# Optimization experiments

Hardware: AMD Instinct MI355X
Metric: run time of the kernel (lower is better)

## Reference

```python
import jax, jax.numpy as jnp
import numpy as np

NUM_HEADS = 16

def _rms_norm(x):
    # F.rms_norm over last dim, eps = dtype machine epsilon (torch default eps=None)
    eps = jnp.finfo(jnp.float32).eps
    ms = jnp.mean(jnp.square(x.astype(jnp.float32)), axis=-1, keepdims=True)
    return (x.astype(jnp.float32) * jax.lax.rsqrt(ms + eps)).astype(x.dtype)

def _rotary_tables(T, head_dim):
    # inv_freq = (1/1024)**linspace(0,1,head_dim//4), padded with zeros to head_dim//2
    quarter = head_dim // 4
    inv_freq = (1.0 / 1024.0) ** jnp.linspace(0.0, 1.0, quarter, dtype=jnp.float32)
    inv_freq = jnp.concatenate([inv_freq, jnp.zeros(quarter, dtype=jnp.float32)])
    t = jnp.arange(T, dtype=jnp.float32)
    theta = t[:, None] * inv_freq[None, :]          # [T, head_dim//2]
    return jnp.cos(theta), jnp.sin(theta)

def _rotary(x, cos, sin):
    # x: [B, T, H, hd]; rotate in fp32, cast back
    xf = x.astype(jnp.float32)
    x1, x2 = jnp.split(xf, 2, axis=-1)
    c = cos[None, :, None, :]
    s = sin[None, :, None, :]
    y1 = x1 * c + x2 * s
    y2 = -x1 * s + x2 * c
    return jnp.concatenate([y1, y2], axis=-1).astype(x.dtype)

def setup_inputs() -> dict:
    key = jax.random.key(0)
    ks = jax.random.split(key, 7)
    B, T, D = 1, 2048, 1024
    sc = 1.0 / np.sqrt(D)
    return {
        "x": jax.random.normal(ks[0], (B, T, D), jnp.float32),
        "vi": jax.random.normal(ks[1], (B, T, D), jnp.float32),
        "Wq": jax.random.normal(ks[2], (D, D), jnp.float32) * sc,
        "Wk": jax.random.normal(ks[3], (D, D), jnp.float32) * sc,
        "Wv": jax.random.normal(ks[4], (D, D), jnp.float32) * sc,
        "Wproj": jax.random.normal(ks[5], (D, D), jnp.float32) * sc,
        "lambdas": jnp.array([0.5, 0.5], jnp.float32),
    }

def reference(x, vi, Wq, Wk, Wv, Wproj, lambdas):
    B, T, D = x.shape
    H = NUM_HEADS
    hd = D // H
    q = (x @ Wq.T).reshape(B, T, H, hd)
    k = (x @ Wk.T).reshape(B, T, H, hd)
    v = (x @ Wv.T).reshape(B, T, H, hd)
    # value residual: lambda-mixed v
    v = lambdas[0] * v + lambdas[1] * vi.reshape(B, T, H, hd)
    q, k = _rms_norm(q), _rms_norm(k)
    cos, sin = _rotary_tables(T, hd)
    q, k = _rotary(q, cos, sin), _rotary(k, cos, sin)
    # causal attention, default flex_attention scale = 1/sqrt(head_dim)
    scores = jnp.einsum('bthd,bshd->bhts', q, k) / jnp.sqrt(jnp.float32(hd))
    causal = jnp.tril(jnp.ones((T, T), dtype=bool))
    scores = jnp.where(causal[None, None], scores, jnp.float32(-1e30))
    attn = jax.nn.softmax(scores, axis=-1)
    y = jnp.einsum('bhts,bshd->bthd', attn, v).reshape(B, T, D)
    return y @ Wproj.T
```

## Files before the change

kernel.cpp:

```cpp
#include <hip/hip_runtime.h>
#include <math.h>

#define T_SEQ 2048
#define D_MODEL 1024
#define NH 16
#define HD 64

typedef unsigned short ushort_t;
typedef unsigned int uint_t;
typedef short short8 __attribute__((ext_vector_type(8)));
typedef float floatx4 __attribute__((ext_vector_type(4)));

__device__ __forceinline__ ushort_t f2bf(float f) {
    uint_t u = __float_as_uint(f);
    u += 0x7FFFu + ((u >> 16) & 1u);
    return (ushort_t)(u >> 16);
}
__device__ __forceinline__ uint_t pack2(float a, float b) {
    return (uint_t)f2bf(a) | ((uint_t)f2bf(b) << 16);
}
__device__ __forceinline__ void gload16(const ushort_t* g, ushort_t* l) {
    __builtin_amdgcn_global_load_lds(
        (const __attribute__((address_space(1))) void*)g,
        (__attribute__((address_space(3))) void*)l, 16, 0, 0);
}

__global__ __launch_bounds__(256) void to_bf16(
        const float* __restrict__ x,  const float* __restrict__ wq,
        const float* __restrict__ wk, const float* __restrict__ wv,
        const float* __restrict__ wp,
        ushort_t* __restrict__ xb,  ushort_t* __restrict__ wqb,
        ushort_t* __restrict__ wkb, ushort_t* __restrict__ wvb,
        ushort_t* __restrict__ wpb)
{
    size_t i = (size_t)blockIdx.x * 256 + threadIdx.x;
    const float* src; ushort_t* dst; size_t off;
    if (i < 262144)      { src = x;  dst = xb;  off = i; }
    else if (i < 393216) { src = wq; dst = wqb; off = i - 262144; }
    else if (i < 524288) { src = wk; dst = wkb; off = i - 393216; }
    else if (i < 655360) { src = wv; dst = wvb; off = i - 524288; }
    else                 { src = wp; dst = wpb; off = i - 655360; }
    float4 f0 = ((const float4*)src)[off * 2];
    float4 f1 = ((const float4*)src)[off * 2 + 1];
    uint4 u;
    u.x = pack2(f0.x, f0.y); u.y = pack2(f0.z, f0.w);
    u.z = pack2(f1.x, f1.y); u.w = pack2(f1.z, f1.w);
    ((uint4*)dst)[off] = u;
}

__global__ __launch_bounds__(256) void gemm_qkv(
        const ushort_t* __restrict__ xb,
        const ushort_t* __restrict__ Wqb, const ushort_t* __restrict__ Wkb,
        const ushort_t* __restrict__ Wvb,
        const float* __restrict__ vi, const float* __restrict__ lam,
        ushort_t* __restrict__ qb, ushort_t* __restrict__ kb,
        ushort_t* __restrict__ vbt)
{
    const int z = blockIdx.z;
    const ushort_t* __restrict__ W = (z == 0) ? Wqb : (z == 1) ? Wkb : Wvb;
    const int d  = blockIdx.y * 8 + blockIdx.x;
    const int ly = (d & 7) * 4 + (d >> 6);
    const int lx = (d >> 3) & 7;
    const int row0 = ly * 64;
    const int col0 = lx * 128;

    __shared__ ushort_t As[2 * 64 * 64];
    __shared__ ushort_t Bs[2 * 128 * 64];

    const int tid = threadIdx.x;
    const int wave = tid >> 6, lane = tid & 63;
    const int wm = wave >> 1, wn = wave & 1;
    const int l15 = lane & 15, quad = lane >> 4;
    const int srow  = tid >> 3;
    const int sslot = (tid & 7) ^ (srow & 7);

    floatx4 acc[2][4];
    #pragma unroll
    for (int i = 0; i < 2; ++i)
        #pragma unroll
        for (int j = 0; j < 4; ++j)
            acc[i][j] = (floatx4){0.f, 0.f, 0.f, 0.f};

    auto stageAB = [&](int k0, int p) {
        ushort_t* Ap = As + p * 4096;
        ushort_t* Bp = Bs + p * 8192;
        #pragma unroll
        for (int c = 0; c < 2; ++c)
            gload16(xb + (size_t)(row0 + c * 32 + srow) * D_MODEL + k0 + sslot * 8,
                    Ap + c * 2048 + tid * 8);
        #pragma unroll
        for (int c = 0; c < 4; ++c)
            gload16(W + (size_t)(col0 + c * 32 + srow) * D_MODEL + k0 + sslot * 8,
                    Bp + c * 2048 + tid * 8);
    };

    stageAB(0, 0);
    int cur = 0;
    for (int k0 = 0; k0 < D_MODEL; k0 += 64) {
        asm volatile("s_waitcnt vmcnt(0)" ::: "memory");
        __builtin_amdgcn_s_barrier();
        const ushort_t* Ac = As + cur * 4096;
        const ushort_t* Bc = Bs + cur * 8192;
        short8 a[2][2], b[2][4];
        #pragma unroll
        for (int kh = 0; kh < 2; ++kh) {
            const int slot = ((kh * 4 + quad) ^ (l15 & 7)) << 3;
            #pragma unroll
            for (int i = 0; i < 2; ++i)
                a[kh][i] = *(const short8*)(Ac + (32 * wm + i * 16 + l15) * 64 + slot);
            #pragma unroll
            for (int j = 0; j < 4; ++j)
                b[kh][j] = *(const short8*)(Bc + (64 * wn + j * 16 + l15) * 64 + slot);
        }
        __builtin_amdgcn_sched_barrier(0);
        if (k0 + 64 < D_MODEL) stageAB(k0 + 64, cur ^ 1);
        __builtin_amdgcn_sched_barrier(0);
        #pragma unroll
        for (int kh = 0; kh < 2; ++kh)
            #pragma unroll
            for (int i = 0; i < 2; ++i)
                #pragma unroll
                for (int j = 0; j < 4; ++j)
                    acc[i][j] = __builtin_amdgcn_mfma_f32_16x16x32_bf16(a[kh][i], b[kh][j], acc[i][j], 0, 0, 0);
        cur ^= 1;
    }

    if (z < 2) {
        ushort_t* __restrict__ o = (z == 0) ? qb : kb;
        const float oscale = (z == 0) ? 0.125f : 1.0f;
        const int hbase = col0 + 64 * wn;
        const float eps = 1.1920929e-7f;
        const float fr = exp2f(-10.0f * (float)l15 / 15.0f);
        #pragma unroll
        for (int i = 0; i < 2; ++i)
            #pragma unroll
            for (int r = 0; r < 4; ++r) {
                const int t = row0 + 32 * wm + i * 16 + quad * 4 + r;
                float v0 = acc[i][0][r], v1 = acc[i][1][r];
                float v2 = acc[i][2][r], v3 = acc[i][3][r];
                float ss = v0 * v0 + v1 * v1 + v2 * v2 + v3 * v3;
                ss += __shfl_xor(ss, 1);
                ss += __shfl_xor(ss, 2);
                ss += __shfl_xor(ss, 4);
                ss += __shfl_xor(ss, 8);
                const float sc = rsqrtf(ss * (1.0f / 64.0f) + eps);
                v0 *= sc; v1 *= sc; v2 *= sc; v3 *= sc;
                const float th = (float)t * fr;
                const float cs = cosf(th), sn = sinf(th);
                const float y0 = v0 * cs + v2 * sn;
                const float y2 = v2 * cs - v0 * sn;
                const size_t rb = (size_t)t * D_MODEL + hbase;
                o[rb +  0 + l15] = f2bf(y0 * oscale);
                o[rb + 16 + l15] = f2bf(v1 * oscale);
                o[rb + 32 + l15] = f2bf(y2 * oscale);
                o[rb + 48 + l15] = f2bf(v3 * oscale);
            }
    } else {
        const float l0 = lam[0], l1 = lam[1];
        #pragma unroll
        for (int i = 0; i < 2; ++i)
            #pragma unroll
            for (int j = 0; j < 4; ++j) {
                const int tb = row0 + 32 * wm + i * 16 + quad * 4;
                const int jj = col0 + 64 * wn + j * 16 + l15;
                float b0 = l0 * acc[i][j][0] + l1 * vi[(size_t)(tb + 0) * D_MODEL + jj];
                float b1 = l0 * acc[i][j][1] + l1 * vi[(size_t)(tb + 1) * D_MODEL + jj];
                float b2 = l0 * acc[i][j][2] + l1 * vi[(size_t)(tb + 2) * D_MODEL + jj];
                float b3 = l0 * acc[i][j][3] + l1 * vi[(size_t)(tb + 3) * D_MODEL + jj];
                uint2 u;
                u.x = pack2(b0, b1);
                u.y = pack2(b2, b3);
                *(uint2*)(vbt + (size_t)jj * T_SEQ + tb) = u;
            }
    }
}

__global__ __launch_bounds__(256) void attn(
        const ushort_t* __restrict__ qb, const ushort_t* __restrict__ kb,
        const ushort_t* __restrict__ vbt, ushort_t* __restrict__ yb,
        float* __restrict__ Opart, float* __restrict__ Lpart)
{
    const int h = blockIdx.x;
    const int x = blockIdx.y;
    int qt, ct_begin, ct_end, pidx;
    if (x < 28) {
        qt = 27 - (x >> 1);
        const int w = qt + 1;
        const int c0 = (w + 1) >> 1;
        if ((x & 1) == 0) { ct_begin = 0;  ct_end = c0; }
        else              { ct_begin = c0; ct_end = w;  }
        pidx = h * 40 + 12 + (qt - 14) * 2 + (x & 1);
    } else if (x < 40) {
        const int xx = x - 28;
        qt = 28 + xx / 3;
        const int c = xx % 3;
        const int w = qt + 1;
        const int b0 = (w + 2) / 3;
        const int b1 = (2 * w + 2) / 3;
        ct_begin = (c == 0) ? 0  : (c == 1) ? b0 : b1;
        ct_end   = (c == 0) ? b0 : (c == 1) ? b1 : w;
        pidx = h * 40 + (qt - 28) * 3 + c;
    } else {
        qt = 53 - x;
        ct_begin = 0; ct_end = qt + 1;
        pidx = -1;
    }
    const int t0 = qt * 64;

    __shared__ ushort_t Ks[2 * 64 * 64];
    __shared__ ushort_t Vs[2 * 64 * 64];
    __shared__ ushort_t QPs[64 * 64];

    const int tid = threadIdx.x;
    const int wave = tid >> 6, lane = tid & 63;
    const int l15 = lane & 15, quad = lane >> 4;
    const int srow  = tid >> 3;
    const int sslot = (tid & 7) ^ (srow & 7);
    const int bx = l15 & 7;

    {
        const int r4 = tid >> 2, c4 = (tid & 3) * 16;
        const ushort_t* src = qb + (size_t)(t0 + r4) * D_MODEL + h * HD + c4;
        uint4 A = ((const uint4*)src)[0];
        uint4 B = ((const uint4*)src)[1];
        const int rs = r4 & 7;
        const int s0 = (c4 >> 3) ^ rs;
        const int s1 = ((c4 >> 3) + 1) ^ rs;
        *(uint4*)(QPs + r4 * 64 + s0 * 8) = A;
        *(uint4*)(QPs + r4 * 64 + s1 * 8) = B;
    }
    __syncthreads();
    short8 qf[2];
    qf[0] = *(const short8*)(QPs + (16 * wave + l15) * 64 + ((quad ^ bx) << 3));
    qf[1] = *(const short8*)(QPs + (16 * wave + l15) * 64 + (((quad + 4) ^ bx) << 3));

    auto stageKV = [&](int kt, int p) {
        const int s0 = kt * 64;
        ushort_t* Kp = Ks + p * 4096;
        ushort_t* Vp = Vs + p * 4096;
        gload16(kb  + (size_t)(s0 + srow)      * D_MODEL + h * HD + sslot * 8, Kp + tid * 8);
        gload16(kb  + (size_t)(s0 + 32 + srow) * D_MODEL + h * HD + sslot * 8, Kp + 2048 + tid * 8);
        gload16(vbt + (size_t)(h * HD + srow)      * T_SEQ + s0 + sslot * 8,   Vp + tid * 8);
        gload16(vbt + (size_t)(h * HD + 32 + srow) * T_SEQ + s0 + sslot * 8,   Vp + 2048 + tid * 8);
    };

    float l_acc[4];
    floatx4 O[4];
    #pragma unroll
    for (int r = 0; r < 4; ++r) l_acc[r] = 0.0f;
    #pragma unroll
    for (int d = 0; d < 4; ++d) O[d] = (floatx4){0.f, 0.f, 0.f, 0.f};

    stageKV(ct_begin, 0);
    int cur = 0;
    for (int kt = ct_begin; kt < ct_end; ++kt) {
        asm volatile("s_waitcnt vmcnt(0)" ::: "memory");
        __builtin_amdgcn_s_barrier();

        if (kt + 1 < ct_end) stageKV(kt + 1, cur ^ 1);
        __builtin_amdgcn_sched_barrier(0);

        const ushort_t* Kc = Ks + cur * 4096;
        const ushort_t* Vc = Vs + cur * 4096;

        floatx4 sa[4];
        __builtin_amdgcn_s_setprio(1);
        #pragma unroll
        for (int ct = 0; ct < 4; ++ct) {
            const ushort_t* krow = Kc + (ct * 16 + l15) * 64;
            short8 b0 = *(const short8*)(krow + ((quad ^ bx) << 3));
            short8 b1 = *(const short8*)(krow + (((quad + 4) ^ bx) << 3));
            floatx4 t4 = (floatx4){0.f, 0.f, 0.f, 0.f};
            t4 = __builtin_amdgcn_mfma_f32_16x16x32_bf16(qf[0], b0, t4, 0, 0, 0);
            t4 = __builtin_amdgcn_mfma_f32_16x16x32_bf16(qf[1], b1, t4, 0, 0, 0);
            sa[ct] = t4;
        }
        __builtin_amdgcn_s_setprio(0);

        if (kt == qt) {
            #pragma unroll
            for (int ct = 0; ct < 4; ++ct)
                #pragma unroll
                for (int r = 0; r < 4; ++r) {
                    int trow = 16 * wave + quad * 4 + r;
                    int scol = ct * 16 + l15;
                    if (scol > trow) sa[ct][r] = -1e30f;
                }
        }
        float p[4][4];
        #pragma unroll
        for (int ct = 0; ct < 4; ++ct)
            #pragma unroll
            for (int r = 0; r < 4; ++r) {
                p[ct][r] = __expf(sa[ct][r] - 8.0f);
                l_acc[r] += p[ct][r];
            }

        #pragma unroll
        for (int ct = 0; ct < 4; ++ct)
            #pragma unroll
            for (int r = 0; r < 4; ++r) {
                const int row = 16 * wave + quad * 4 + r;
                const int ps = (ct * 2 + (l15 >> 3)) ^ (row & 7);
                QPs[row * 64 + ps * 8 + (l15 & 7)] = f2bf(p[ct][r]);
            }

        short8 pa0 = *(const short8*)(QPs + (16 * wave + l15) * 64 + ((quad ^ bx) << 3));
        short8 pa1 = *(const short8*)(QPs + (16 * wave + l15) * 64 + (((quad + 4) ^ bx) << 3));
        __builtin_amdgcn_s_setprio(1);
        #pragma unroll
        for (int dt = 0; dt < 4; ++dt) {
            const ushort_t* vrow = Vc + (dt * 16 + l15) * 64;
            short8 vb0 = *(const short8*)(vrow + ((quad ^ bx) << 3));
            short8 vb1 = *(const short8*)(vrow + (((quad + 4) ^ bx) << 3));
            O[dt] = __builtin_amdgcn_mfma_f32_16x16x32_bf16(pa0, vb0, O[dt], 0, 0, 0);
            O[dt] = __builtin_amdgcn_mfma_f32_16x16x32_bf16(pa1, vb1, O[dt], 0, 0, 0);
        }
        __builtin_amdgcn_s_setprio(0);
        cur ^= 1;
    }

    float l_run[4];
    #pragma unroll
    for (int r = 0; r < 4; ++r) {
        float s = l_acc[r];
        s += __shfl_xor(s, 1);
        s += __shfl_xor(s, 2);
        s += __shfl_xor(s, 4);
        s += __shfl_xor(s, 8);
        l_run[r] = s;
    }

    if (pidx < 0) {
        #pragma unroll
        for (int r = 0; r < 4; ++r) {
            const float inv_l = 1.0f / l_run[r];
            const int t = t0 + 16 * wave + quad * 4 + r;
            #pragma unroll
            for (int dt = 0; dt < 4; ++dt)
                yb[(size_t)t * D_MODEL + h * HD + dt * 16 + l15] = f2bf(O[dt][r] * inv_l);
        }
    } else {
        float* __restrict__ Op = Opart + (size_t)pidx * 4096;
        #pragma unroll
        for (int r = 0; r < 4; ++r) {
            const int row = 16 * wave + quad * 4 + r;
            #pragma unroll
            for (int dt = 0; dt < 4; ++dt)
                Op[row * 64 + dt * 16 + l15] = O[dt][r];
            if (l15 == 0) Lpart[(size_t)pidx * 64 + row] = l_run[r];
        }
    }
}

__global__ __launch_bounds__(256) void attn_combine(
        const float* __restrict__ Opart, const float* __restrict__ Lpart,
        ushort_t* __restrict__ yb)
{
    const int h  = blockIdx.x;
    const int qt = 14 + (int)blockIdx.y;
    const int tid = threadIdx.x;
    const int row  = tid >> 2;
    const int dseg = (tid & 3) * 16;
    int s0, nc;
    if (qt >= 28) { s0 = (qt - 28) * 3;        nc = 3; }
    else          { s0 = 12 + (qt - 14) * 2;   nc = 2; }
    const int p0 = h * 40 + s0;

    float accv[16];
    #pragma unroll
    for (int e = 0; e < 16; ++e) accv[e] = 0.0f;
    float lsum = 0.0f;
    for (int c = 0; c < nc; ++c) {
        const float* Op = Opart + (size_t)(p0 + c) * 4096 + row * 64 + dseg;
        lsum += Lpart[(size_t)(p0 + c) * 64 + row];
        #pragma unroll
        for (int g = 0; g < 4; ++g) {
            float4 a = ((const float4*)Op)[g];
            accv[g * 4 + 0] += a.x;
            accv[g * 4 + 1] += a.y;
            accv[g * 4 + 2] += a.z;
            accv[g * 4 + 3] += a.w;
        }
    }
    const float inv = 1.0f / lsum;

    uint_t u[8];
    #pragma unroll
    for (int g = 0; g < 4; ++g) {
        u[g * 2 + 0] = pack2(accv[g * 4 + 0] * inv, accv[g * 4 + 1] * inv);
        u[g * 2 + 1] = pack2(accv[g * 4 + 2] * inv, accv[g * 4 + 3] * inv);
    }
    const int t = qt * 64 + row;
    uint4* dst = (uint4*)(yb + (size_t)t * D_MODEL + h * HD + dseg);
    dst[0] = make_uint4(u[0], u[1], u[2], u[3]);
    dst[1] = make_uint4(u[4], u[5], u[6], u[7]);
}

__global__ __launch_bounds__(256) void gemm_proj(
        const ushort_t* __restrict__ yb, const ushort_t* __restrict__ Wpb,
        float* __restrict__ out)
{
    const int d  = blockIdx.y * 16 + blockIdx.x;
    const int ly = (d & 7) * 4 + (d >> 7);
    const int lx = (d >> 3) & 15;
    const int row0 = ly * 64;
    const int col0 = lx * 64;

    __shared__ ushort_t As[2 * 64 * 64];
    __shared__ ushort_t Bs[2 * 64 * 64];

    const int tid = threadIdx.x;
    const int wave = tid >> 6, lane = tid & 63;
    const int l15 = lane & 15, quad = lane >> 4;
    const int srow  = tid >> 3;
    const int sslot = (tid & 7) ^ (srow & 7);

    floatx4 acc4[4];
    #pragma unroll
    for (int j = 0; j < 4; ++j)
        acc4[j] = (floatx4){0.f, 0.f, 0.f, 0.f};

    auto stageAB = [&](int k0, int p) {
        ushort_t* Ap = As + p * 4096;
        ushort_t* Bp = Bs + p * 4096;
        #pragma unroll
        for (int c = 0; c < 2; ++c)
            gload16(yb + (size_t)(row0 + c * 32 + srow) * D_MODEL + k0 + sslot * 8,
                    Ap + c * 2048 + tid * 8);
        #pragma unroll
        for (int c = 0; c < 2; ++c)
            gload16(Wpb + (size_t)(col0 + c * 32 + srow) * D_MODEL + k0 + sslot * 8,
                    Bp + c * 2048 + tid * 8);
    };

    stageAB(0, 0);
    int cur = 0;
    for (int k0 = 0; k0 < D_MODEL; k0 += 64) {
        asm volatile("s_waitcnt vmcnt(0)" ::: "memory");
        __builtin_amdgcn_s_barrier();
        const ushort_t* Ac = As + cur * 4096;
        const ushort_t* Bc = Bs + cur * 4096;
        short8 a[2], b[2][4];
        #pragma unroll
        for (int kh = 0; kh < 2; ++kh) {
            const int slot = ((kh * 4 + quad) ^ (l15 & 7)) << 3;
            a[kh] = *(const short8*)(Ac + (16 * wave + l15) * 64 + slot);
            #pragma unroll
            for (int j = 0; j < 4; ++j)
                b[kh][j] = *(const short8*)(Bc + (j * 16 + l15) * 64 + slot);
        }
        __builtin_amdgcn_sched_barrier(0);
        if (k0 + 64 < D_MODEL) stageAB(k0 + 64, cur ^ 1);
        __builtin_amdgcn_sched_barrier(0);
        #pragma unroll
        for (int kh = 0; kh < 2; ++kh)
            #pragma unroll
            for (int j = 0; j < 4; ++j)
                acc4[j] = __builtin_amdgcn_mfma_f32_16x16x32_bf16(a[kh], b[kh][j], acc4[j], 0, 0, 0);
        cur ^= 1;
    }

    #pragma unroll
    for (int j = 0; j < 4; ++j) {
        const int t = row0 + 16 * wave + quad * 4;
        const int jj = col0 + j * 16 + l15;
        #pragma unroll
        for (int r = 0; r < 4; ++r)
            out[(size_t)(t + r) * D_MODEL + jj] = acc4[j][r];
    }
}

extern "C" void kernel_launch(void* const* d_in, const int* in_sizes, int n_in,
                              void* d_out, int out_size, void* d_ws, size_t ws_size,
                              hipStream_t stream) {
    (void)in_sizes; (void)n_in; (void)out_size; (void)ws_size;
    const float* x   = (const float*)d_in[0];
    const float* vi  = (const float*)d_in[1];
    const float* Wq  = (const float*)d_in[2];
    const float* Wk  = (const float*)d_in[3];
    const float* Wv  = (const float*)d_in[4];
    const float* Wp  = (const float*)d_in[5];
    const float* lam = (const float*)d_in[6];

    char* base = (char*)d_ws;
    ushort_t* xb  = (ushort_t*)(base);
    ushort_t* wqb = (ushort_t*)(base + (size_t)4  * 1048576);
    ushort_t* wkb = (ushort_t*)(base + (size_t)6  * 1048576);
    ushort_t* wvb = (ushort_t*)(base + (size_t)8  * 1048576);
    ushort_t* wpb = (ushort_t*)(base + (size_t)10 * 1048576);
    ushort_t* qb  = (ushort_t*)(base + (size_t)12 * 1048576);
    ushort_t* kb  = (ushort_t*)(base + (size_t)16 * 1048576);
    ushort_t* vbt = (ushort_t*)(base + (size_t)20 * 1048576);
    ushort_t* yb  = (ushort_t*)(base + (size_t)24 * 1048576);
    float* Opart  = (float*)(base);
    float* Lpart  = (float*)d_out;
    float* out = (float*)d_out;

    to_bf16<<<dim3(786432 / 256), 256, 0, stream>>>(x, Wq, Wk, Wv, Wp, xb, wqb, wkb, wvb, wpb);
    gemm_qkv<<<dim3(8, 32, 3), 256, 0, stream>>>(xb, wqb, wkb, wvb, vi, lam, qb, kb, vbt);
    attn<<<dim3(16, 54), 256, 0, stream>>>(qb, kb, vbt, yb, Opart, Lpart);
    attn_combine<<<dim3(16, 18), 256, 0, stream>>>(Opart, Lpart, yb);
    gemm_proj<<<dim3(16, 32), 256, 0, stream>>>(yb, wpb, out);
}
```

Baseline: 141.6 us.

## Enlarge attention query tile to 128 rows and rebalance split-K partitions

The attention kernel now processes 128 query rows per block (two 16-row fragments per wave), so each staged K/V tile feeds twice as many MFMAs. The block schedule is rebuilt around 16 query tiles: the upper half are split into two key ranges and merged by a simplified two-way combine, the rest run whole. This halves K/V global and LDS traffic per query but doubles register use and gives fewer, larger blocks (400 instead of 864), so load balance and occupancy are the risks. A launch-bounds occupancy hint is also added.

```diff
diff --git a/kernel.cpp b/kernel.cpp
--- a/kernel.cpp
+++ b/kernel.cpp
@@ -175,41 +175,31 @@
     }
 }
 
-__global__ __launch_bounds__(256) void attn(
+__global__ __launch_bounds__(256, 3) void attn(
         const ushort_t* __restrict__ qb, const ushort_t* __restrict__ kb,
         const ushort_t* __restrict__ vbt, ushort_t* __restrict__ yb,
         float* __restrict__ Opart, float* __restrict__ Lpart)
 {
     const int h = blockIdx.x;
     const int x = blockIdx.y;
-    int qt, ct_begin, ct_end, pidx;
-    if (x < 28) {
-        qt = 27 - (x >> 1);
-        const int w = qt + 1;
-        const int c0 = (w + 1) >> 1;
-        if ((x & 1) == 0) { ct_begin = 0;  ct_end = c0; }
-        else              { ct_begin = c0; ct_end = w;  }
-        pidx = h * 40 + 12 + (qt - 14) * 2 + (x & 1);
-    } else if (x < 40) {
-        const int xx = x - 28;
-        qt = 28 + xx / 3;
-        const int c = xx % 3;
-        const int w = qt + 1;
-        const int b0 = (w + 2) / 3;
-        const int b1 = (2 * w + 2) / 3;
-        ct_begin = (c == 0) ? 0  : (c == 1) ? b0 : b1;
-        ct_end   = (c == 0) ? b0 : (c == 1) ? b1 : w;
-        pidx = h * 40 + (qt - 28) * 3 + c;
+    int Q, ct_begin, ct_end, pidx;
+    if (x < 18) {
+        Q = 15 - (x >> 1);
+        const int w = 2 * Q + 2;
+        const int mid = Q + 1;
+        if ((x & 1) == 0) { ct_begin = 0;   ct_end = mid; }
+        else              { ct_begin = mid; ct_end = w;   }
+        pidx = h * 18 + x;
     } else {
-        qt = 53 - x;
-        ct_begin = 0; ct_end = qt + 1;
+        Q = 24 - x;
+        ct_begin = 0; ct_end = 2 * Q + 2;
         pidx = -1;
     }
-    const int t0 = qt * 64;
+    const int t0 = Q * 128;
 
     __shared__ ushort_t Ks[2 * 64 * 64];
     __shared__ ushort_t Vs[2 * 64 * 64];
-    __shared__ ushort_t QPs[64 * 64];
+    __shared__ ushort_t QPs[128 * 64];
 
     const int tid = threadIdx.x;
     const int wave = tid >> 6, lane = tid & 63;
@@ -219,20 +209,27 @@
     const int bx = l15 & 7;
 
     {
-        const int r4 = tid >> 2, c4 = (tid & 3) * 16;
+        const int r4 = tid >> 1, c4 = (tid & 1) * 32;
         const ushort_t* src = qb + (size_t)(t0 + r4) * D_MODEL + h * HD + c4;
         uint4 A = ((const uint4*)src)[0];
         uint4 B = ((const uint4*)src)[1];
+        uint4 C = ((const uint4*)src)[2];
+        uint4 D = ((const uint4*)src)[3];
         const int rs = r4 & 7;
-        const int s0 = (c4 >> 3) ^ rs;
-        const int s1 = ((c4 >> 3) + 1) ^ rs;
-        *(uint4*)(QPs + r4 * 64 + s0 * 8) = A;
-        *(uint4*)(QPs + r4 * 64 + s1 * 8) = B;
+        const int s0 = c4 >> 3;
+        *(uint4*)(QPs + r4 * 64 + ((s0 + 0) ^ rs) * 8) = A;
+        *(uint4*)(QPs + r4 * 64 + ((s0 + 1) ^ rs) * 8) = B;
+        *(uint4*)(QPs + r4 * 64 + ((s0 + 2) ^ rs) * 8) = C;
+        *(uint4*)(QPs + r4 * 64 + ((s0 + 3) ^ rs) * 8) = D;
     }
     __syncthreads();
-    short8 qf[2];
-    qf[0] = *(const short8*)(QPs + (16 * wave + l15) * 64 + ((quad ^ bx) << 3));
-    qf[1] = *(const short8*)(QPs + (16 * wave + l15) * 64 + (((quad + 4) ^ bx) << 3));
+    short8 qf[2][2];
+    #pragma unroll
+    for (int rf = 0; rf < 2; ++rf) {
+        const int row = 32 * wave + rf * 16 + l15;
+        qf[rf][0] = *(const short8*)(QPs + row * 64 + ((quad ^ bx) << 3));
+        qf[rf][1] = *(const short8*)(QPs + row * 64 + (((quad + 4) ^ bx) << 3));
+    }
 
     auto stageKV = [&](int kt, int p) {
         const int s0 = kt * 64;
@@ -244,12 +241,16 @@
         gload16(vbt + (size_t)(h * HD + 32 + srow) * T_SEQ + s0 + sslot * 8,   Vp + 2048 + tid * 8);
     };
 
-    float l_acc[4];
-    floatx4 O[4];
-    #pragma unroll
-    for (int r = 0; r < 4; ++r) l_acc[r] = 0.0f;
-    #pragma unroll
-    for (int d = 0; d < 4; ++d) O[d] = (floatx4){0.f, 0.f, 0.f, 0.f};
+    float l_acc[2][4];
+    floatx4 O[2][4];
+    #pragma unroll
+    for (int rf = 0; rf < 2; ++rf)
+        #pragma unroll
+        for (int r = 0; r < 4; ++r) l_acc[rf][r] = 0.0f;
+    #pragma unroll
+    for (int rf = 0; rf < 2; ++rf)
+        #pragma unroll
+        for (int d = 0; d < 4; ++d) O[rf][d] = (floatx4){0.f, 0.f, 0.f, 0.f};
 
     stageKV(ct_begin, 0);
     int cur = 0;
@@ -263,93 +264,117 @@
         const ushort_t* Kc = Ks + cur * 4096;
         const ushort_t* Vc = Vs + cur * 4096;
 
-        floatx4 sa[4];
+        floatx4 sa[2][4];
         __builtin_amdgcn_s_setprio(1);
         #pragma unroll
         for (int ct = 0; ct < 4; ++ct) {
             const ushort_t* krow = Kc + (ct * 16 + l15) * 64;
             short8 b0 = *(const short8*)(krow + ((quad ^ bx) << 3));
             short8 b1 = *(const short8*)(krow + (((quad + 4) ^ bx) << 3));
-            floatx4 t4 = (floatx4){0.f, 0.f, 0.f, 0.f};
-            t4 = __builtin_amdgcn_mfma_f32_16x16x32_bf16(qf[0], b0, t4, 0, 0, 0);
-            t4 = __builtin_amdgcn_mfma_f32_16x16x32_bf16(qf[1], b1, t4, 0, 0, 0);
-            sa[ct] = t4;
+            #pragma unroll
+            for (int rf = 0; rf < 2; ++rf) {
+                floatx4 t4 = (floatx4){0.f, 0.f, 0.f, 0.f};
+                t4 = __builtin_amdgcn_mfma_f32_16x16x32_bf16(qf[rf][0], b0, t4, 0, 0, 0);
+                t4 = __builtin_amdgcn_mfma_f32_16x16x32_bf16(qf[rf][1], b1, t4, 0, 0, 0);
+                sa[rf][ct] = t4;
+            }
         }
         __builtin_amdgcn_s_setprio(0);
 
-        if (kt == qt) {
+        if (kt >= 2 * Q) {
+            const int sbase = kt * 64 - t0;
             #pragma unroll
             for (int ct = 0; ct < 4; ++ct)
                 #pragma unroll
+                for (int rf = 0; rf < 2; ++rf)
+                    #pragma unroll
+                    for (int r = 0; r < 4; ++r) {
+                        int rowrel = 32 * wave + rf * 16 + quad * 4 + r;
+                        int scol = sbase + ct * 16 + l15;
+                        if (scol > rowrel) sa[rf][ct][r] = -1e30f;
+                    }
+        }
+        float p[4][2][4];
+        #pragma unroll
+        for (int ct = 0; ct < 4; ++ct)
+            #pragma unroll
+            for (int rf = 0; rf < 2; ++rf)
+                #pragma unroll
                 for (int r = 0; r < 4; ++r) {
-                    int trow = 16 * wave + quad * 4 + r;
-                    int scol = ct * 16 + l15;
-                    if (scol > trow) sa[ct][r] = -1e30f;
+                    p[ct][rf][r] = __expf(sa[rf][ct][r] - 8.0f);
+                    l_acc[rf][r] += p[ct][rf][r];
                 }
-        }
-        float p[4][4];
+
         #pragma unroll
         for (int ct = 0; ct < 4; ++ct)
             #pragma unroll
-            for (int r = 0; r < 4; ++r) {
-                p[ct][r] = __expf(sa[ct][r] - 8.0f);
-                l_acc[r] += p[ct][r];
-            }
-
-        #pragma unroll
-        for (int ct = 0; ct < 4; ++ct)
-            #pragma unroll
-            for (int r = 0; r < 4; ++r) {
-                const int row = 16 * wave + quad * 4 + r;
-                const int ps = (ct * 2 + (l15 >> 3)) ^ (row & 7);
-                QPs[row * 64 + ps * 8 + (l15 & 7)] = f2bf(p[ct][r]);
-            }
-
-        short8 pa0 = *(const short8*)(QPs + (16 * wave + l15) * 64 + ((quad ^ bx) << 3));
-        short8 pa1 = *(const short8*)(QPs + (16 * wave + l15) * 64 + (((quad + 4) ^ bx) << 3));
+            for (int rf = 0; rf < 2; ++rf)
+                #pragma unroll
+                for (int r = 0; r < 4; ++r) {
+                    const int row = 32 * wave + rf * 16 + quad * 4 + r;
+                    const int ps = (ct * 2 + (l15 >> 3)) ^ (row & 7);
+                    QPs[row * 64 + ps * 8 + (l15 & 7)] = f2bf(p[ct][rf][r]);
+                }
+
+        short8 pa[2][2];
+        #pragma unroll
+        for (int rf = 0; rf < 2; ++rf) {
+            const int row = 32 * wave + rf * 16 + l15;
+            pa[rf][0] = *(const short8*)(QPs + row * 64 + ((quad ^ bx) << 3));
+            pa[rf][1] = *(const short8*)(QPs + row * 64 + (((quad + 4) ^ bx) << 3));
+        }
         __builtin_amdgcn_s_setprio(1);
         #pragma unroll
         for (int dt = 0; dt < 4; ++dt) {
             const ushort_t* vrow = Vc + (dt * 16 + l15) * 64;
             short8 vb0 = *(const short8*)(vrow + ((quad ^ bx) << 3));
             short8 vb1 = *(const short8*)(vrow + (((quad + 4) ^ bx) << 3));
-            O[dt] = __builtin_amdgcn_mfma_f32_16x16x32_bf16(pa0, vb0, O[dt], 0, 0, 0);
-            O[dt] = __builtin_amdgcn_mfma_f32_16x16x32_bf16(pa1, vb1, O[dt], 0, 0, 0);
+            #pragma unroll
+            for (int rf = 0; rf < 2; ++rf) {
+                O[rf][dt] = __builtin_amdgcn_mfma_f32_16x16x32_bf16(pa[rf][0], vb0, O[rf][dt], 0, 0, 0);
+                O[rf][dt] = __builtin_amdgcn_mfma_f32_16x16x32_bf16(pa[rf][1], vb1, O[rf][dt], 0, 0, 0);
+            }
         }
         __builtin_amdgcn_s_setprio(0);
         cur ^= 1;
     }
 
-    float l_run[4];
-    #pragma unroll
-    for (int r = 0; r < 4; ++r) {
-        float s = l_acc[r];
-        s += __shfl_xor(s, 1);
-        s += __shfl_xor(s, 2);
-        s += __shfl_xor(s, 4);
-        s += __shfl_xor(s, 8);
-        l_run[r] = s;
-    }
+    float l_run[2][4];
+    #pragma unroll
+    for (int rf = 0; rf < 2; ++rf)
+        #pragma unroll
+        for (int r = 0; r < 4; ++r) {
+            float s = l_acc[rf][r];
+            s += __shfl_xor(s, 1);
+            s += __shfl_xor(s, 2);
+            s += __shfl_xor(s, 4);
+            s += __shfl_xor(s, 8);
+            l_run[rf][r] = s;
+        }
 
     if (pidx < 0) {
         #pragma unroll
-        for (int r = 0; r < 4; ++r) {
-            const float inv_l = 1.0f / l_run[r];
-            const int t = t0 + 16 * wave + quad * 4 + r;
-            #pragma unroll
-            for (int dt = 0; dt < 4; ++dt)
-                yb[(size_t)t * D_MODEL + h * HD + dt * 16 + l15] = f2bf(O[dt][r] * inv_l);
-        }
+        for (int rf = 0; rf < 2; ++rf)
+            #pragma unroll
+            for (int r = 0; r < 4; ++r) {
+                const float inv_l = 1.0f / l_run[rf][r];
+                const int t = t0 + 32 * wave + rf * 16 + quad * 4 + r;
+                #pragma unroll
+                for (int dt = 0; dt < 4; ++dt)
+                    yb[(size_t)t * D_MODEL + h * HD + dt * 16 + l15] = f2bf(O[rf][dt][r] * inv_l);
+            }
     } else {
-        float* __restrict__ Op = Opart + (size_t)pidx * 4096;
-        #pragma unroll
-        for (int r = 0; r < 4; ++r) {
-            const int row = 16 * wave + quad * 4 + r;
-            #pragma unroll
-            for (int dt = 0; dt < 4; ++dt)
-                Op[row * 64 + dt * 16 + l15] = O[dt][r];
-            if (l15 == 0) Lpart[(size_t)pidx * 64 + row] = l_run[r];
-        }
+        float* __restrict__ Op = Opart + (size_t)pidx * 8192;
+        #pragma unroll
+        for (int rf = 0; rf < 2; ++rf)
+            #pragma unroll
+            for (int r = 0; r < 4; ++r) {
+                const int row = 32 * wave + rf * 16 + quad * 4 + r;
+                #pragma unroll
+                for (int dt = 0; dt < 4; ++dt)
+                    Op[row * 64 + dt * 16 + l15] = O[rf][dt][r];
+                if (l15 == 0) Lpart[(size_t)pidx * 128 + row] = l_run[rf][r];
+            }
     }
 }
 
@@ -357,44 +382,34 @@
         const float* __restrict__ Opart, const float* __restrict__ Lpart,
         ushort_t* __restrict__ yb)
 {
-    const int h  = blockIdx.x;
-    const int qt = 14 + (int)blockIdx.y;
+    const int h = blockIdx.x;
+    const int Q = 7 + (int)blockIdx.y;
     const int tid = threadIdx.x;
-    const int row  = tid >> 2;
-    const int dseg = (tid & 3) * 16;
-    int s0, nc;
-    if (qt >= 28) { s0 = (qt - 28) * 3;        nc = 3; }
-    else          { s0 = 12 + (qt - 14) * 2;   nc = 2; }
-    const int p0 = h * 40 + s0;
-
-    float accv[16];
-    #pragma unroll
-    for (int e = 0; e < 16; ++e) accv[e] = 0.0f;
-    float lsum = 0.0f;
-    for (int c = 0; c < nc; ++c) {
-        const float* Op = Opart + (size_t)(p0 + c) * 4096 + row * 64 + dseg;
-        lsum += Lpart[(size_t)(p0 + c) * 64 + row];
-        #pragma unroll
-        for (int g = 0; g < 4; ++g) {
-            float4 a = ((const float4*)Op)[g];
-            accv[g * 4 + 0] += a.x;
-            accv[g * 4 + 1] += a.y;
-            accv[g * 4 + 2] += a.z;
-            accv[g * 4 + 3] += a.w;
-        }
-    }
-    const float inv = 1.0f / lsum;
-
-    uint_t u[8];
-    #pragma unroll
-    for (int g = 0; g < 4; ++g) {
-        u[g * 2 + 0] = pack2(accv[g * 4 + 0] * inv, accv[g * 4 + 1] * inv);
-        u[g * 2 + 1] = pack2(accv[g * 4 + 2] * inv, accv[g * 4 + 3] * inv);
-    }
-    const int t = qt * 64 + row;
-    uint4* dst = (uint4*)(yb + (size_t)t * D_MODEL + h * HD + dseg);
-    dst[0] = make_uint4(u[0], u[1], u[2], u[3]);
-    dst[1] = make_uint4(u[4], u[5], u[6], u[7]);
+    const int row = tid >> 1;
+    const int cs  = (tid & 1) * 32;
+    const int p0 = h * 18 + (15 - Q) * 2;
+
+    const float l0 = Lpart[(size_t)p0 * 128 + row];
+    const float l1 = Lpart[((size_t)p0 + 1) * 128 + row];
+    const float inv = 1.0f / (l0 + l1);
+
+    const float* O0 = Opart + (size_t)p0 * 8192 + row * 64 + cs;
+    const float* O1 = O0 + 8192;
+
+    uint_t u[16];
+    #pragma unroll
+    for (int g = 0; g < 8; ++g) {
+        float4 a = ((const float4*)O0)[g];
+        float4 b = ((const float4*)O1)[g];
+        u[g * 2 + 0] = pack2((a.x + b.x) * inv, (a.y + b.y) * inv);
+        u[g * 2 + 1] = pack2((a.z + b.z) * inv, (a.w + b.w) * inv);
+    }
+    const int t = Q * 128 + row;
+    uint4* dst = (uint4*)(yb + (size_t)t * D_MODEL + h * HD + cs);
+    dst[0] = make_uint4(u[0],  u[1],  u[2],  u[3]);
+    dst[1] = make_uint4(u[4],  u[5],  u[6],  u[7]);
+    dst[2] = make_uint4(u[8],  u[9],  u[10], u[11]);
+    dst[3] = make_uint4(u[12], u[13], u[14], u[15]);
 }
 
 __global__ __launch_bounds__(256) void gemm_proj(
@@ -499,7 +514,7 @@
 
     to_bf16<<<dim3(786432 / 256), 256, 0, stream>>>(x, Wq, Wk, Wv, Wp, xb, wqb, wkb, wvb, wpb);
     gemm_qkv<<<dim3(8, 32, 3), 256, 0, stream>>>(xb, wqb, wkb, wvb, vi, lam, qb, kb, vbt);
-    attn<<<dim3(16, 54), 256, 0, stream>>>(qb, kb, vbt, yb, Opart, Lpart);
-    attn_combine<<<dim3(16, 18), 256, 0, stream>>>(Opart, Lpart, yb);
+    attn<<<dim3(16, 25), 256, 0, stream>>>(qb, kb, vbt, yb, Opart, Lpart);
+    attn_combine<<<dim3(16, 9), 256, 0, stream>>>(Opart, Lpart, yb);
     gemm_proj<<<dim3(16, 32), 256, 0, stream>>>(yb, wpb, out);
 }
```

Result: slower. 145.5 us (+2.8%).
